# Kernel optimization log

Hardware: AMD Instinct MI355X
Metric: run time of the kernel (lower is better)

Reference implementation:

```python
import jax, jax.numpy as jnp
import numpy as np

B = 8       # complexes in batch
C = 32      # CDR residues per antibody
G = 2048    # antigen nodes per complex
D = 128     # encoded_dims
N_AB = B * C
N_AG = B * G
N = N_AB + N_AG
SLOPE = 0.2
EPS_BN = 1e-5


def _build_edges():
    # block-sparse bipartite edges (cdr_b x ag_b), symmetrized, + self loops
    srcs, dsts = [], []
    for b in range(B):
        ab = np.arange(b * C, (b + 1) * C)
        ag = np.arange(N_AB + b * G, N_AB + (b + 1) * G)
        g1, g2 = np.meshgrid(ab, ag, indexing='ij')
        srcs.append(g1.ravel()); dsts.append(g2.ravel())
    s = np.concatenate(srcs); d = np.concatenate(dsts)
    loops = np.arange(N)
    src = np.concatenate([s, d, loops]).astype(np.int32)
    dst = np.concatenate([d, s, loops]).astype(np.int32)
    return src, dst


def setup_inputs() -> dict:
    key = jax.random.key(0)
    ks = jax.random.split(key, 16)
    sc = 1.0 / np.sqrt(D)
    edge_src, edge_dst = _build_edges()
    return {
        'selected_ab': jax.random.normal(ks[0], (N_AB, D), jnp.float32),
        'x_ag': jax.random.normal(ks[1], (N_AG, D), jnp.float32),
        'W1': jax.random.normal(ks[2], (D, D), jnp.float32) * sc,
        'a_src1': jax.random.normal(ks[3], (D,), jnp.float32) * sc,
        'a_dst1': jax.random.normal(ks[4], (D,), jnp.float32) * sc,
        'b1': jnp.zeros((D,), jnp.float32),
        'W2': jax.random.normal(ks[5], (D, D), jnp.float32) * sc,
        'a_src2': jax.random.normal(ks[6], (D,), jnp.float32) * sc,
        'a_dst2': jax.random.normal(ks[7], (D,), jnp.float32) * sc,
        'b2': jnp.zeros((D,), jnp.float32),
        'bn_ab_g': jnp.ones((2 * D,), jnp.float32),
        'bn_ab_b': jnp.zeros((2 * D,), jnp.float32),
        'bn_ag_g': jnp.ones((2 * D,), jnp.float32),
        'bn_ag_b': jnp.zeros((2 * D,), jnp.float32),
        'fc_w': jax.random.normal(ks[8], (2 * D, 1), jnp.float32) * sc,
        'fc_b': jnp.zeros((1,), jnp.float32),
        'agfc_w': jax.random.normal(ks[9], (2 * D, 1), jnp.float32) * sc,
        'agfc_b': jnp.zeros((1,), jnp.float32),
        'edge_src': jnp.asarray(edge_src),
        'edge_dst': jnp.asarray(edge_dst),
    }


def _gat(x, W, a_s, a_d, b, src, dst):
    # PyG GATConv, heads=1, eval mode (dropout off)
    h = x @ W                                  # [N, D]
    al_s = h @ a_s                             # [N]
    al_d = h @ a_d                             # [N]
    e = jax.nn.leaky_relu(al_s[src] + al_d[dst], SLOPE)   # [E]
    m = jax.ops.segment_max(e, dst, num_segments=N)
    e = jnp.exp(e - m[dst])
    z = jax.ops.segment_sum(e, dst, num_segments=N)
    alpha = e / (z[dst] + 1e-16)
    out = jax.ops.segment_sum(h[src] * alpha[:, None], dst, num_segments=N)
    return out + b


def _bn(x, g, b):
    # training-mode batch stats (biased variance), like torch BatchNorm1d
    m = x.mean(0)
    v = ((x - m) ** 2).mean(0)
    return (x - m) / jnp.sqrt(v + EPS_BN) * g + b


def reference(selected_ab, x_ag, W1, a_src1, a_dst1, b1, W2, a_src2, a_dst2, b2,
              bn_ab_g, bn_ab_b, bn_ag_g, bn_ag_b, fc_w, fc_b, agfc_w, agfc_b,
              edge_src, edge_dst):
    x = jnp.concatenate([selected_ab, x_ag], axis=0)          # [N, D]
    x = jax.nn.relu(_gat(x, W1, a_src1, a_dst1, b1, edge_src, edge_dst))
    x = _gat(x, W2, a_src2, a_dst2, b2, edge_src, edge_dst)
    x_ab = jnp.concatenate([x[:N_AB], selected_ab], axis=1)   # [N_ab, 2D]
    x_ab = jax.nn.relu(_bn(x_ab, bn_ab_g, bn_ab_b))
    x_ab = (x_ab @ fc_w + fc_b).ravel()
    x_ag_o = jnp.concatenate([x[N_AB:], x_ag], axis=1)        # [N_ag, 2D]
    x_ag_o = jax.nn.relu(_bn(x_ag_o, bn_ag_g, bn_ag_b))
    x_ag_o = (x_ag_o @ agfc_w + agfc_b).ravel()
    return (x_ab, x_ag_o)
```

## Files before the change

kernel.cpp:

```cpp
#include <hip/hip_runtime.h>


#define N_AB 256
#define N_AG 16384
#define N_ALL 16640
#define G_AG 2048
#define SLOPE 0.2f
#define MSHIFT 20.0f

typedef __attribute__((ext_vector_type(4))) float f32x4;
typedef __attribute__((ext_vector_type(8))) __bf16 bf16x8;
typedef __attribute__((ext_vector_type(8))) unsigned short u16x8;
typedef unsigned short ushort_t;

__device__ __forceinline__ float bf2f(ushort_t u) {
  union { unsigned int i; float f; } v; v.i = ((unsigned int)u) << 16; return v.f;
}
__device__ __forceinline__ ushort_t f2bf(float f) {
  union { float fv; unsigned int i; } v; v.fv = f;
  unsigned int x = v.i;
  return (ushort_t)((x + 0x7fffu + ((x >> 16) & 1u)) >> 16);
}
__device__ __forceinline__ float lrelu(float x) { return x >= 0.f ? x : SLOPE * x; }
__device__ __forceinline__ float expw(float e) {
  return __expf(fminf(e, 60.f) - MSHIFT);
}
__device__ __forceinline__ float ldf(const void* p, size_t i, int f) {
  return f ? ((const float*)p)[i] : bf2f(((const ushort_t*)p)[i]);
}
__device__ __forceinline__ void ld8f(const void* p, size_t i, int f, float* o) {
  if (f) {
    const f32x4* q = (const f32x4*)((const float*)p + i);
    f32x4 a = q[0], b = q[1];
#pragma unroll
    for (int j = 0; j < 4; ++j) { o[j] = a[j]; o[j + 4] = b[j]; }
  } else {
    u16x8 v = *(const u16x8*)((const ushort_t*)p + i);
#pragma unroll
    for (int j = 0; j < 8; ++j) o[j] = bf2f(v[j]);
  }
}

__global__ __launch_bounds__(256) void k_pre(
    const void* __restrict__ W1, const void* __restrict__ W2,
    const void* __restrict__ as1, const void* __restrict__ ad1,
    const void* __restrict__ as2, const void* __restrict__ ad2,
    const ushort_t* __restrict__ selu,
    ushort_t* __restrict__ W1t, ushort_t* __restrict__ W2t,
    float* __restrict__ va, float* __restrict__ bnsumAG,
    float* __restrict__ accf, float* __restrict__ accz,
    int* __restrict__ flagp) {
  int t = threadIdx.x, lane = t & 63, wid = t >> 6;
  int bx = blockIdx.x;
  int cnt = 0;
#pragma unroll
  for (int i = 0; i < 8; ++i) {
    unsigned e = (selu[lane * 8 + i] >> 7) & 0xFF;
    if (e > 0xC8) cnt++;
  }
  int f = (__popcll(__ballot(cnt > 0)) >= 3) ? 1 : 0;
  if (bx == 0 && t == 0) flagp[0] = f;

  if (bx < 16) {
    const void* W = (bx < 8) ? W1 : W2;
    ushort_t* Wt = (bx < 8) ? W1t : W2t;
    int base = (bx & 7) * 2048 + t * 8;
    float o[8];
    ld8f(W, base, f, o);
#pragma unroll
    for (int j = 0; j < 8; ++j) {
      int idx = base + j;
      Wt[(idx & 127) * 128 + (idx >> 7)] = f2bf(o[j]);
    }
  } else if (bx < 32) {
    int j = bx - 16;
    const void* W   = (j < 8) ? W1 : W2;
    const void* asv = (j < 8) ? as1 : as2;
    const void* adv = (j < 8) ? ad1 : ad2;
    int vbase = (j < 8) ? 0 : 256;
    int basek = (j & 7) * 16 + wid * 4;
    float a_s0 = ldf(asv, lane, f), a_s1 = ldf(asv, lane + 64, f);
    float a_d0 = ldf(adv, lane, f), a_d1 = ldf(adv, lane + 64, f);
#pragma unroll
    for (int i = 0; i < 4; ++i) {
      int k = basek + i;
      float w0 = ldf(W, (size_t)k * 128 + lane, f);
      float w1 = ldf(W, (size_t)k * 128 + lane + 64, f);
      float ps = w0 * a_s0 + w1 * a_s1;
      float pd = w0 * a_d0 + w1 * a_d1;
#pragma unroll
      for (int o = 1; o < 64; o <<= 1) {
        ps += __shfl_xor(ps, o);
        pd += __shfl_xor(pd, o);
      }
      if (lane == 0) { va[vbase + k] = ps; va[vbase + 128 + k] = pd; }
    }
  } else {
    int j = bx - 32;
    f32x4* az = (f32x4*)(accf + (size_t)j * 4096);
    f32x4 z4 = (f32x4){0.f, 0.f, 0.f, 0.f};
    for (int i = t; i < 1024; i += 256) az[i] = z4;
    if (j == 0) { bnsumAG[t] = 0.f; bnsumAG[t + 256] = 0.f; accz[t] = 0.f; }
  }
}

__global__ __launch_bounds__(256) void k_gemm(
    const void* __restrict__ xa, int modeA,
    const void* __restrict__ xb, int modeB,
    const int* __restrict__ flagp,
    const ushort_t* __restrict__ Wt, const float* __restrict__ va,
    ushort_t* __restrict__ h, float* __restrict__ als, float* __restrict__ ald) {
  int lane = threadIdx.x & 63, wid = threadIdx.x >> 6;
  int rw0 = blockIdx.x * 64 + wid * 16;
  const void* xsrc; int roff, mode;
  if (rw0 < N_AB) { xsrc = xa; roff = rw0; mode = modeA; }
  else            { xsrc = xb; roff = rw0 - N_AB; mode = modeB; }
  int fx = (mode == 2) ? *flagp : mode;
  int mm = lane & 15, q = lane >> 4;
  f32x4 acc[8];
#pragma unroll
  for (int b = 0; b < 8; ++b) acc[b] = (f32x4){0.f, 0.f, 0.f, 0.f};
  float pals = 0.f, pald = 0.f;
#pragma unroll
  for (int s = 0; s < 4; ++s) {
    int koff = s * 32 + q * 8;
    union { u16x8 u; bf16x8 b; } af;
    float o[8];
    ld8f(xsrc, (size_t)(roff + mm) * 128 + koff, fx, o);
#pragma unroll
    for (int j = 0; j < 8; ++j) {
      af.u[j] = f2bf(o[j]);
      pals += o[j] * va[koff + j];
      pald += o[j] * va[128 + koff + j];
    }
#pragma unroll
    for (int nt = 0; nt < 8; ++nt) {
      bf16x8 bfr = *(const bf16x8*)(Wt + (size_t)(nt * 16 + mm) * 128 + koff);
      acc[nt] = __builtin_amdgcn_mfma_f32_16x16x32_bf16(af.b, bfr, acc[nt], 0, 0, 0);
    }
  }
  {
    float s1 = pals; s1 += __shfl_xor(s1, 16); s1 += __shfl_xor(s1, 32);
    float d1 = pald; d1 += __shfl_xor(d1, 16); d1 += __shfl_xor(d1, 32);
    if (lane < 16) { als[rw0 + lane] = s1; ald[rw0 + lane] = d1; }
  }
#pragma unroll
  for (int nt = 0; nt < 8; ++nt)
#pragma unroll
    for (int r = 0; r < 4; ++r) {
      int row = rw0 + q * 4 + r;
      int col = nt * 16 + mm;
      h[(size_t)row * 128 + col] = f2bf(acc[nt][r]);
    }
}

#define ABP_STRIDE 72
#define AG_STRIDE 40
__global__ __launch_bounds__(256) void k_agg(
    const ushort_t* __restrict__ h, const float* __restrict__ als,
    const float* __restrict__ ald, const void* __restrict__ bias,
    const int* __restrict__ flagp, ushort_t* __restrict__ xout,
    float* __restrict__ accf, float* __restrict__ accz,
    const void* __restrict__ x_ag, float* __restrict__ bnsumAG,
    int do_relu, int do_bnsum) {
  __shared__ ushort_t hT[128 * ABP_STRIDE];
  __shared__ float alsS[64];
  __shared__ float colsum[128], colsq[128];
  int bx = blockIdx.x;
  int t = threadIdx.x, lane = t & 63, wid = t >> 6;
  int mm = lane & 15, q = lane >> 4;

  if (bx < 256) {
    int b = bx >> 5, jt = bx & 31;
    int f = *flagp;
    {
      int row = t & 31, c0 = (t >> 5) * 16;
      const ushort_t* src = h + (size_t)(b * 32 + row) * 128 + c0;
      u16x8 v0 = *(const u16x8*)src;
      u16x8 v1 = *(const u16x8*)(src + 8);
#pragma unroll
      for (int j = 0; j < 8; ++j) {
        hT[(c0 + j) * AG_STRIDE + row] = v0[j];
        hT[(c0 + 8 + j) * AG_STRIDE + row] = v1[j];
      }
      if (t < 32) alsS[t] = als[b * 32 + t];
      if (t < 128) { colsum[t] = 0.f; colsq[t] = 0.f; }
    }
    __syncthreads();
    int jl = jt * 64 + wid * 16;
    int jrow = N_AB + b * G_AG + jl;
    float aldj = ald[jrow + mm];
    float alsj = als[jrow + mm];
    union { u16x8 u; bf16x8 b; } af;
    float zp = 0.f;
#pragma unroll
    for (int j = 0; j < 8; ++j) {
      ushort_t us = f2bf(expw(lrelu(alsS[q * 8 + j] + aldj)));
      af.u[j] = us;
      zp += bf2f(us);
    }
    zp += __shfl_xor(zp, 16);
    zp += __shfl_xor(zp, 32);
    float wself = expw(lrelu(alsj + aldj));
    float z = zp + wself;
#pragma unroll
    for (int nt = 0; nt < 8; ++nt) {
      int col = nt * 16 + mm;
      union { u16x8 u; bf16x8 b; } bfr;
      bfr.b = *(const bf16x8*)(&hT[col * AG_STRIDE + q * 8]);
      f32x4 acc = {0.f, 0.f, 0.f, 0.f};
      acc = __builtin_amdgcn_mfma_f32_16x16x32_bf16(af.b, bfr.b, acc, 0, 0, 0);
      float biasv = ldf(bias, col, f);
      float sl = 0.f, sq = 0.f;
#pragma unroll
      for (int r = 0; r < 4; ++r) {
        int row = q * 4 + r;
        float zr = __shfl(z, row);
        float wsr = __shfl(wself, row);
        float hv = bf2f(h[(size_t)(jrow + row) * 128 + col]);
        float v = (acc[r] + wsr * hv) / (zr + 1e-16f) + biasv;
        sl += v; sq += v * v;
        if (do_relu) v = fmaxf(v, 0.f);
        xout[(size_t)(jrow + row) * 128 + col] = f2bf(v);
      }
      if (do_bnsum) {
        atomicAdd(&colsum[col], sl);
        atomicAdd(&colsq[col], sq);
      }
    }
    if (do_bnsum) {
      __syncthreads();
      if (t < 128) {
        atomicAdd(&bnsumAG[t], colsum[t]);
        atomicAdd(&bnsumAG[256 + t], colsq[t]);
      }
    }
  } else if (bx < 512) {
    int bx2 = bx - 256;
    int b = bx2 >> 5, sg = bx2 & 31;
    int jrow0 = N_AB + b * G_AG + sg * 64;
    {
      int jr = t & 63, cgrp = (t >> 6) * 32;
      const ushort_t* src = h + (size_t)(jrow0 + jr) * 128 + cgrp;
#pragma unroll
      for (int v = 0; v < 4; ++v) {
        u16x8 vv = *(const u16x8*)(src + v * 8);
#pragma unroll
        for (int j = 0; j < 8; ++j)
          hT[(cgrp + v * 8 + j) * ABP_STRIDE + jr] = vv[j];
      }
      if (t < 64) alsS[t] = als[jrow0 + t];
    }
    __syncthreads();
    float aldm[2] = { ald[b * 32 + mm], ald[b * 32 + 16 + mm] };
    f32x4 acc[2][2];
#pragma unroll
    for (int a = 0; a < 2; ++a)
#pragma unroll
      for (int c = 0; c < 2; ++c) acc[a][c] = (f32x4){0.f, 0.f, 0.f, 0.f};
    float zz[2] = {0.f, 0.f};
#pragma unroll
    for (int s = 0; s < 2; ++s) {
      int k0 = s * 32 + q * 8;
      float a8[8];
#pragma unroll
      for (int j = 0; j < 8; ++j) a8[j] = alsS[k0 + j];
      union { u16x8 u; bf16x8 b; } af[2];
#pragma unroll
      for (int mt = 0; mt < 2; ++mt)
#pragma unroll
        for (int j = 0; j < 8; ++j) {
          ushort_t us = f2bf(expw(lrelu(a8[j] + aldm[mt])));
          af[mt].u[j] = us;
          zz[mt] += bf2f(us);
        }
#pragma unroll
      for (int ns = 0; ns < 2; ++ns) {
        int n = wid * 32 + ns * 16 + mm;
        union { u16x8 u; bf16x8 b; } bfr;
        bfr.b = *(const bf16x8*)(&hT[n * ABP_STRIDE + k0]);
        acc[0][ns] = __builtin_amdgcn_mfma_f32_16x16x32_bf16(af[0].b, bfr.b, acc[0][ns], 0, 0, 0);
        acc[1][ns] = __builtin_amdgcn_mfma_f32_16x16x32_bf16(af[1].b, bfr.b, acc[1][ns], 0, 0, 0);
      }
    }
#pragma unroll
    for (int mt = 0; mt < 2; ++mt)
#pragma unroll
      for (int ns = 0; ns < 2; ++ns)
#pragma unroll
        for (int r = 0; r < 4; ++r) {
          int row = b * 32 + mt * 16 + q * 4 + r;
          int col = wid * 32 + ns * 16 + mm;
          atomicAdd(&accf[(size_t)row * 128 + col], acc[mt][ns][r]);
        }
#pragma unroll
    for (int mt = 0; mt < 2; ++mt) {
      float z = zz[mt];
      z += __shfl_xor(z, 16);
      z += __shfl_xor(z, 32);
      if (wid == 0 && lane < 16)
        atomicAdd(&accz[b * 32 + mt * 16 + lane], z);
    }
  } else {
    int j = bx - 512;
    int f = *flagp;
    int col = t & 127, half = t >> 7;
    int r0 = j * 256 + half * 128;
    float s = 0.f, sq = 0.f;
    for (int r = 0; r < 128; ++r) {
      float v = ldf(x_ag, (size_t)(r0 + r) * 128 + col, f);
      s += v; sq += v * v;
    }
    atomicAdd(&bnsumAG[128 + col], s);
    atomicAdd(&bnsumAG[384 + col], sq);
  }
}

__global__ __launch_bounds__(256) void k_abfin(
    float* __restrict__ accf, float* __restrict__ accz,
    const ushort_t* __restrict__ h, const float* __restrict__ als,
    const float* __restrict__ ald, const void* __restrict__ bias,
    const int* __restrict__ flagp, float* __restrict__ xabf, int do_relu) {
  __shared__ float zsh[32];
  int b = blockIdx.x, t = threadIdx.x;
  int f = *flagp;
  if (t < 32) {
    int grow = b * 32 + t;
    float w = expw(lrelu(als[grow] + ald[grow]));
    zsh[t] = accz[grow] + w;
    accz[grow] = 0.f;
  }
  __syncthreads();
  int c = t & 127, rh = t >> 7;
  float biasv = ldf(bias, c, f);
#pragma unroll 4
  for (int r = 0; r < 16; ++r) {
    int row = rh * 16 + r;
    int grow = b * 32 + row;
    float wself = expw(lrelu(als[grow] + ald[grow]));
    size_t idx = (size_t)grow * 128 + c;
    float hv = bf2f(h[idx]);
    float v = (accf[idx] + wself * hv) / (zsh[row] + 1e-16f) + biasv;
    accf[idx] = 0.f;
    if (do_relu) v = fmaxf(v, 0.f);
    xabf[idx] = v;
  }
}

__global__ __launch_bounds__(256) void k_stats(
    const float* __restrict__ xfab, const void* __restrict__ sel_ab,
    const float* __restrict__ bnsumAG,
    const void* __restrict__ gab, const void* __restrict__ bab,
    const void* __restrict__ gag, const void* __restrict__ bag,
    const void* __restrict__ fcw, const void* __restrict__ agfcw,
    const int* __restrict__ flagp,
    float* __restrict__ statsAB, float* __restrict__ statsAG) {
  int c = threadIdx.x;
  int f = *flagp;
  if (blockIdx.x == 0) {
    float s = 0.f, sq = 0.f;
    if (c < 128) {
      for (int r = 0; r < 256; ++r) { float v = xfab[(size_t)r * 128 + c]; s += v; sq += v * v; }
    } else {
      for (int r = 0; r < 256; ++r) {
        float v = ldf(sel_ab, (size_t)r * 128 + (c - 128), f);
        s += v; sq += v * v;
      }
    }
    float mean = s * (1.f / 256.f);
    float var = fmaxf(sq * (1.f / 256.f) - mean * mean, 0.f);
    float A = ldf(gab, c, f) / sqrtf(var + 1e-5f);
    statsAB[c] = A;
    statsAB[256 + c] = ldf(bab, c, f) - mean * A;
    statsAB[512 + c] = ldf(fcw, c, f);
  } else {
    float mean = bnsumAG[c] * (1.f / 16384.f);
    float var = fmaxf(bnsumAG[256 + c] * (1.f / 16384.f) - mean * mean, 0.f);
    float A = ldf(gag, c, f) / sqrtf(var + 1e-5f);
    statsAG[c] = A;
    statsAG[256 + c] = ldf(bag, c, f) - mean * A;
    statsAG[512 + c] = ldf(agfcw, c, f);
  }
}

__global__ __launch_bounds__(256) void k_head(
    const float* __restrict__ xfab, const ushort_t* __restrict__ xfag,
    const void* __restrict__ sel_ab, const void* __restrict__ x_ag,
    const float* __restrict__ statsAB, const float* __restrict__ statsAG,
    const void* __restrict__ fcb, const void* __restrict__ agfcb,
    const int* __restrict__ flagp, void* __restrict__ out) {
  int lane = threadIdx.x & 63, wid = threadIdx.x >> 6;
  int row = blockIdx.x * 4 + wid;
  int f = *flagp;
  int c0 = lane * 2;
  const float* st;
  float v0, v1, v2, v3, bb;
  if (row < N_AB) {
    st = statsAB;
    const float* p = xfab + (size_t)row * 128 + c0;
    v0 = p[0]; v1 = p[1];
    size_t ro = (size_t)row * 128 + c0;
    v2 = ldf(sel_ab, ro, f);
    v3 = ldf(sel_ab, ro + 1, f);
    bb = ldf(fcb, 0, f);
  } else {
    st = statsAG;
    const ushort_t* p = xfag + (size_t)row * 128 + c0;
    v0 = bf2f(p[0]); v1 = bf2f(p[1]);
    size_t ro = (size_t)(row - N_AB) * 128 + c0;
    v2 = ldf(x_ag, ro, f);
    v3 = ldf(x_ag, ro + 1, f);
    bb = ldf(agfcb, 0, f);
  }
  float acc =
      fmaxf(v0 * st[c0]           + st[256 + c0],     0.f) * st[512 + c0]
    + fmaxf(v1 * st[c0 + 1]       + st[256 + c0 + 1], 0.f) * st[512 + c0 + 1]
    + fmaxf(v2 * st[128 + c0]     + st[384 + c0],     0.f) * st[640 + c0]
    + fmaxf(v3 * st[128 + c0 + 1] + st[384 + c0 + 1], 0.f) * st[640 + c0 + 1];
#pragma unroll
  for (int o = 1; o < 64; o <<= 1) acc += __shfl_xor(acc, o);
  if (lane == 0) {
    float r = acc + bb;
    if (f) ((float*)out)[row] = r;
    else   ((ushort_t*)out)[row] = f2bf(r);
  }
}

extern "C" void kernel_launch(void* const* d_in, const int* in_sizes, int n_in,
                              void* d_out, int out_size, void* d_ws, size_t ws_size,
                              hipStream_t stream) {
  (void)in_sizes; (void)n_in; (void)out_size; (void)ws_size;
  const void* sel_ab = d_in[0];
  const void* x_ag   = d_in[1];
  const void* W1     = d_in[2];
  const void* as1    = d_in[3];
  const void* ad1    = d_in[4];
  const void* b1     = d_in[5];
  const void* W2     = d_in[6];
  const void* as2    = d_in[7];
  const void* ad2    = d_in[8];
  const void* b2     = d_in[9];
  const void* gab    = d_in[10];
  const void* bab    = d_in[11];
  const void* gag    = d_in[12];
  const void* bag    = d_in[13];
  const void* fcw    = d_in[14];
  const void* fcb    = d_in[15];
  const void* agfcw  = d_in[16];
  const void* agfcb  = d_in[17];

  ushort_t* h  = (ushort_t*)d_in[18];
  ushort_t* xb = (ushort_t*)d_in[19];

  char* wsp = (char*)d_ws;
  size_t off = 0;
  auto carve = [&](size_t bytes) -> char* {
    char* p = wsp + off; off += (bytes + 255) & ~(size_t)255; return p;
  };
  int* flag      = (int*)carve(64 * 4);
  ushort_t* W1t  = (ushort_t*)carve(16384 * 2);
  ushort_t* W2t  = (ushort_t*)carve(16384 * 2);
  float* va      = (float*)carve(512 * 4);
  float* als     = (float*)carve((size_t)N_ALL * 4);
  float* ald     = (float*)carve((size_t)N_ALL * 4);
  float* bnsumAG = (float*)carve(512 * 4);
  float* statsAB = (float*)carve(768 * 4);
  float* statsAG = (float*)carve(768 * 4);
  float* xabf    = (float*)carve((size_t)N_AB * 128 * 4);
  float* accf    = (float*)carve((size_t)N_AB * 128 * 4);
  float* accz    = (float*)carve(256 * 4);

  k_pre<<<40, 256, 0, stream>>>(W1, W2, as1, ad1, as2, ad2,
                                (const ushort_t*)sel_ab, W1t, W2t, va,
                                bnsumAG, accf, accz, flag);
  k_gemm<<<260, 256, 0, stream>>>(sel_ab, 2, x_ag, 2, flag, W1t, va, h, als, ald);
  k_agg<<<512, 256, 0, stream>>>(h, als, ald, b1, flag, xb, accf, accz,
                                 x_ag, bnsumAG, 1, 0);
  k_abfin<<<8, 256, 0, stream>>>(accf, accz, h, als, ald, b1, flag, xabf, 1);
  k_gemm<<<260, 256, 0, stream>>>(xabf, 1, xb + (size_t)N_AB * 128, 0, flag, W2t, va + 256, h, als, ald);
  k_agg<<<576, 256, 0, stream>>>(h, als, ald, b2, flag, xb, accf, accz,
                                 x_ag, bnsumAG, 0, 1);
  k_abfin<<<8, 256, 0, stream>>>(accf, accz, h, als, ald, b2, flag, xabf, 0);
  k_stats<<<2, 256, 0, stream>>>(xabf, sel_ab, bnsumAG, gab, bab, gag, bag, fcw, agfcw, flag, statsAB, statsAG);
  k_head<<<4160, 256, 0, stream>>>(xabf, xb, sel_ab, x_ag, statsAB, statsAG, fcb, agfcb, flag, d_out);
}
```

Baseline: 199.6 us.

## Replace global atomic accumulation for antibody rows with partial buffers and reduction

The antibody-side aggregation blocks now write per-segment partial sums (numerator and normalizer) to dedicated buffers instead of issuing global float atomicAdds into a shared accumulator. The finalize kernel sums the 32 partials per row, and its grid grows from 8 to 32 blocks. The x_ag column-statistics pass moves from the second aggregation launch into the preprocessing kernel, and a memset replaces the in-kernel zeroing. This removes atomic contention and the zero-reset traffic, at the cost of extra partial-buffer writes and reads (about 4 MB).

```diff
diff --git a/kernel.cpp b/kernel.cpp
--- a/kernel.cpp
+++ b/kernel.cpp
@@ -45,10 +45,9 @@
     const void* __restrict__ W1, const void* __restrict__ W2,
     const void* __restrict__ as1, const void* __restrict__ ad1,
     const void* __restrict__ as2, const void* __restrict__ ad2,
-    const ushort_t* __restrict__ selu,
+    const ushort_t* __restrict__ selu, const void* __restrict__ x_ag,
     ushort_t* __restrict__ W1t, ushort_t* __restrict__ W2t,
     float* __restrict__ va, float* __restrict__ bnsumAG,
-    float* __restrict__ accf, float* __restrict__ accz,
     int* __restrict__ flagp) {
   int t = threadIdx.x, lane = t & 63, wid = t >> 6;
   int bx = blockIdx.x;
@@ -97,10 +96,15 @@
     }
   } else {
     int j = bx - 32;
-    f32x4* az = (f32x4*)(accf + (size_t)j * 4096);
-    f32x4 z4 = (f32x4){0.f, 0.f, 0.f, 0.f};
-    for (int i = t; i < 1024; i += 256) az[i] = z4;
-    if (j == 0) { bnsumAG[t] = 0.f; bnsumAG[t + 256] = 0.f; accz[t] = 0.f; }
+    int col = t & 127, half = t >> 7;
+    int r0 = j * 256 + half * 128;
+    float s = 0.f, sq = 0.f;
+    for (int r = 0; r < 128; ++r) {
+      float v = ldf(x_ag, (size_t)(r0 + r) * 128 + col, f);
+      s += v; sq += v * v;
+    }
+    atomicAdd(&bnsumAG[128 + col], s);
+    atomicAdd(&bnsumAG[384 + col], sq);
   }
 }
 
@@ -160,12 +164,11 @@
     const ushort_t* __restrict__ h, const float* __restrict__ als,
     const float* __restrict__ ald, const void* __restrict__ bias,
     const int* __restrict__ flagp, ushort_t* __restrict__ xout,
-    float* __restrict__ accf, float* __restrict__ accz,
-    const void* __restrict__ x_ag, float* __restrict__ bnsumAG,
-    int do_relu, int do_bnsum) {
+    float* __restrict__ part_d, float* __restrict__ part_z,
+    float* __restrict__ bnsumAG, int do_relu, int do_bnsum) {
   __shared__ ushort_t hT[128 * ABP_STRIDE];
   __shared__ float alsS[64];
-  __shared__ float colsum[128], colsq[128];
+  __shared__ float cs0[128], cs1[128];
   int bx = blockIdx.x;
   int t = threadIdx.x, lane = t & 63, wid = t >> 6;
   int mm = lane & 15, q = lane >> 4;
@@ -174,17 +177,17 @@
     int b = bx >> 5, jt = bx & 31;
     int f = *flagp;
     {
-      int row = t & 31, c0 = (t >> 5) * 16;
-      const ushort_t* src = h + (size_t)(b * 32 + row) * 128 + c0;
+      int row = t & 31, c0g = (t >> 5) * 16;
+      const ushort_t* src = h + (size_t)(b * 32 + row) * 128 + c0g;
       u16x8 v0 = *(const u16x8*)src;
       u16x8 v1 = *(const u16x8*)(src + 8);
 #pragma unroll
       for (int j = 0; j < 8; ++j) {
-        hT[(c0 + j) * AG_STRIDE + row] = v0[j];
-        hT[(c0 + 8 + j) * AG_STRIDE + row] = v1[j];
+        hT[(c0g + j) * AG_STRIDE + row] = v0[j];
+        hT[(c0g + 8 + j) * AG_STRIDE + row] = v1[j];
       }
       if (t < 32) alsS[t] = als[b * 32 + t];
-      if (t < 128) { colsum[t] = 0.f; colsq[t] = 0.f; }
+      if (t < 128) { cs0[t] = 0.f; cs1[t] = 0.f; }
     }
     __syncthreads();
     int jl = jt * 64 + wid * 16;
@@ -224,18 +227,18 @@
         xout[(size_t)(jrow + row) * 128 + col] = f2bf(v);
       }
       if (do_bnsum) {
-        atomicAdd(&colsum[col], sl);
-        atomicAdd(&colsq[col], sq);
+        atomicAdd(&cs0[col], sl);
+        atomicAdd(&cs1[col], sq);
       }
     }
     if (do_bnsum) {
       __syncthreads();
       if (t < 128) {
-        atomicAdd(&bnsumAG[t], colsum[t]);
-        atomicAdd(&bnsumAG[256 + t], colsq[t]);
-      }
-    }
-  } else if (bx < 512) {
+        atomicAdd(&bnsumAG[t], cs0[t]);
+        atomicAdd(&bnsumAG[256 + t], cs1[t]);
+      }
+    }
+  } else {
     int bx2 = bx - 256;
     int b = bx2 >> 5, sg = bx2 & 31;
     int jrow0 = N_AB + b * G_AG + sg * 64;
@@ -283,15 +286,16 @@
         acc[1][ns] = __builtin_amdgcn_mfma_f32_16x16x32_bf16(af[1].b, bfr.b, acc[1][ns], 0, 0, 0);
       }
     }
+    float* pd = part_d + (size_t)(b * 32 + sg) * 32 * 128;
 #pragma unroll
     for (int mt = 0; mt < 2; ++mt)
 #pragma unroll
       for (int ns = 0; ns < 2; ++ns)
 #pragma unroll
         for (int r = 0; r < 4; ++r) {
-          int row = b * 32 + mt * 16 + q * 4 + r;
+          int rowl = mt * 16 + q * 4 + r;
           int col = wid * 32 + ns * 16 + mm;
-          atomicAdd(&accf[(size_t)row * 128 + col], acc[mt][ns][r]);
+          pd[rowl * 128 + col] = acc[mt][ns][r];
         }
 #pragma unroll
     for (int mt = 0; mt < 2; ++mt) {
@@ -299,49 +303,42 @@
       z += __shfl_xor(z, 16);
       z += __shfl_xor(z, 32);
       if (wid == 0 && lane < 16)
-        atomicAdd(&accz[b * 32 + mt * 16 + lane], z);
-    }
-  } else {
-    int j = bx - 512;
-    int f = *flagp;
-    int col = t & 127, half = t >> 7;
-    int r0 = j * 256 + half * 128;
-    float s = 0.f, sq = 0.f;
-    for (int r = 0; r < 128; ++r) {
-      float v = ldf(x_ag, (size_t)(r0 + r) * 128 + col, f);
-      s += v; sq += v * v;
-    }
-    atomicAdd(&bnsumAG[128 + col], s);
-    atomicAdd(&bnsumAG[384 + col], sq);
+        part_z[(size_t)(b * 32 + sg) * 32 + mt * 16 + lane] = z;
+    }
   }
 }
 
 __global__ __launch_bounds__(256) void k_abfin(
-    float* __restrict__ accf, float* __restrict__ accz,
+    const float* __restrict__ part_d, const float* __restrict__ part_z,
     const ushort_t* __restrict__ h, const float* __restrict__ als,
     const float* __restrict__ ald, const void* __restrict__ bias,
     const int* __restrict__ flagp, float* __restrict__ xabf, int do_relu) {
-  __shared__ float zsh[32];
-  int b = blockIdx.x, t = threadIdx.x;
+  __shared__ float zsh[8], wsh[8];
+  int bx = blockIdx.x, t = threadIdx.x;
+  int b = bx >> 2, q4 = bx & 3;
   int f = *flagp;
-  if (t < 32) {
-    int grow = b * 32 + t;
+  if (t < 8) {
+    int rowb = q4 * 8 + t;
+    int grow = b * 32 + rowb;
     float w = expw(lrelu(als[grow] + ald[grow]));
-    zsh[t] = accz[grow] + w;
-    accz[grow] = 0.f;
+    float z = w;
+    for (int sg = 0; sg < 32; ++sg)
+      z += part_z[(size_t)(b * 32 + sg) * 32 + rowb];
+    zsh[t] = z; wsh[t] = w;
   }
   __syncthreads();
-  int c = t & 127, rh = t >> 7;
-  float biasv = ldf(bias, c, f);
-#pragma unroll 4
-  for (int r = 0; r < 16; ++r) {
-    int row = rh * 16 + r;
-    int grow = b * 32 + row;
-    float wself = expw(lrelu(als[grow] + ald[grow]));
-    size_t idx = (size_t)grow * 128 + c;
+#pragma unroll
+  for (int i = 0; i < 4; ++i) {
+    int e = i * 256 + t;
+    int rl = e >> 7, col = e & 127;
+    int rowb = q4 * 8 + rl;
+    int grow = b * 32 + rowb;
+    float acc = 0.f;
+    for (int sg = 0; sg < 32; ++sg)
+      acc += part_d[((size_t)(b * 32 + sg) * 32 + rowb) * 128 + col];
+    size_t idx = (size_t)grow * 128 + col;
     float hv = bf2f(h[idx]);
-    float v = (accf[idx] + wself * hv) / (zsh[row] + 1e-16f) + biasv;
-    accf[idx] = 0.f;
+    float v = (acc + wsh[rl] * hv) / (zsh[rl] + 1e-16f) + ldf(bias, col, f);
     if (do_relu) v = fmaxf(v, 0.f);
     xabf[idx] = v;
   }
@@ -467,20 +464,21 @@
   float* statsAB = (float*)carve(768 * 4);
   float* statsAG = (float*)carve(768 * 4);
   float* xabf    = (float*)carve((size_t)N_AB * 128 * 4);
-  float* accf    = (float*)carve((size_t)N_AB * 128 * 4);
-  float* accz    = (float*)carve(256 * 4);
-
-  k_pre<<<40, 256, 0, stream>>>(W1, W2, as1, ad1, as2, ad2,
-                                (const ushort_t*)sel_ab, W1t, W2t, va,
-                                bnsumAG, accf, accz, flag);
+  float* part_d  = (float*)carve((size_t)256 * 32 * 128 * 4);
+  float* part_z  = (float*)carve((size_t)256 * 32 * 4);
+
+  hipMemsetAsync(bnsumAG, 0, 512 * 4, stream);
+  k_pre<<<96, 256, 0, stream>>>(W1, W2, as1, ad1, as2, ad2,
+                                (const ushort_t*)sel_ab, x_ag,
+                                W1t, W2t, va, bnsumAG, flag);
   k_gemm<<<260, 256, 0, stream>>>(sel_ab, 2, x_ag, 2, flag, W1t, va, h, als, ald);
-  k_agg<<<512, 256, 0, stream>>>(h, als, ald, b1, flag, xb, accf, accz,
-                                 x_ag, bnsumAG, 1, 0);
-  k_abfin<<<8, 256, 0, stream>>>(accf, accz, h, als, ald, b1, flag, xabf, 1);
+  k_agg<<<512, 256, 0, stream>>>(h, als, ald, b1, flag, xb, part_d, part_z,
+                                 bnsumAG, 1, 0);
+  k_abfin<<<32, 256, 0, stream>>>(part_d, part_z, h, als, ald, b1, flag, xabf, 1);
   k_gemm<<<260, 256, 0, stream>>>(xabf, 1, xb + (size_t)N_AB * 128, 0, flag, W2t, va + 256, h, als, ald);
-  k_agg<<<576, 256, 0, stream>>>(h, als, ald, b2, flag, xb, accf, accz,
-                                 x_ag, bnsumAG, 0, 1);
-  k_abfin<<<8, 256, 0, stream>>>(accf, accz, h, als, ald, b2, flag, xabf, 0);
+  k_agg<<<512, 256, 0, stream>>>(h, als, ald, b2, flag, xb, part_d, part_z,
+                                 bnsumAG, 0, 1);
+  k_abfin<<<32, 256, 0, stream>>>(part_d, part_z, h, als, ald, b2, flag, xabf, 0);
   k_stats<<<2, 256, 0, stream>>>(xabf, sel_ab, bnsumAG, gab, bab, gag, bag, fcw, agfcw, flag, statsAB, statsAG);
   k_head<<<4160, 256, 0, stream>>>(xabf, xb, sel_ab, x_ag, statsAB, statsAG, fcb, agfcb, flag, d_out);
 }
```

After: 212.2 us. 1.06x slower.
